# Performance work log

Measured on AMD Instinct MI355X. Metric: run time of the kernel, lower is better.

## Reference

```python
import jax, jax.numpy as jnp
import numpy as np

B, S, E, H = 8, 2048, 512, 4
D = E // H


def setup_inputs() -> dict:
    key = jax.random.key(0)
    ks = jax.random.split(key, 9)
    std = 0.05  # keras 'normal' initializer default stddev
    return {
        "x": jax.random.normal(ks[0], (B, S, E), dtype=jnp.float32),
        "Wq": jax.random.normal(ks[1], (E, E), dtype=jnp.float32) * std,
        "Wk": jax.random.normal(ks[2], (E, E), dtype=jnp.float32) * std,
        "Wv": jax.random.normal(ks[3], (E, E), dtype=jnp.float32) * std,
        "Wepi": jax.random.normal(ks[4], (S, S), dtype=jnp.float32) * std,
        "bq": jax.random.normal(ks[5], (S, 1), dtype=jnp.float32) * std,
        "bk": jax.random.normal(ks[6], (S, 1), dtype=jnp.float32) * std,
        "bv": jax.random.normal(ks[7], (S, 1), dtype=jnp.float32) * std,
        "bo": jax.random.normal(ks[8], (S, 1), dtype=jnp.float32) * std,
    }


def reference(x, Wq, Wk, Wv, Wepi, bq, bk, bv, bo):
    b, s, e = x.shape
    # QKV projections; [S,1] biases broadcast across the feature dim
    q = x @ Wq + bq  # [B,S,E]
    k = x @ Wk + bk
    v = x @ Wv + bv
    # split heads -> [B,H,S,D]
    q = q.reshape(b, s, H, D).transpose(0, 2, 1, 3)
    k = k.reshape(b, s, H, D).transpose(0, 2, 1, 3)
    v = v.reshape(b, s, H, D).transpose(0, 2, 1, 3)
    # NOTE: source scales by sqrt(seq_length), not sqrt(head_dim)
    scale = 1.0 / np.sqrt(float(s)).astype(np.float32)
    scores = jnp.einsum("bhsd,bhtd->bhst", q, k) * scale  # [B,H,S,S]
    attn = jax.nn.softmax(scores, axis=-1)
    # epigenomic multiplicative mask applied AFTER softmax (broadcast [S,S])
    attn = attn * Wepi
    effect = jnp.einsum("bhst,bhtd->bhsd", attn, v)  # [B,H,S,D]
    effect = effect.transpose(0, 2, 1, 3).reshape(b, s, e) + bo
    # original returns attention in merged-batch layout [B*H, S, S]
    return effect, attn.reshape(b * H, s, s)
```

## Files before the change

kernel.cpp:

```cpp
#include <hip/hip_runtime.h>
#include <hip/hip_bf16.h>

constexpr int Bn = 8, Sn = 2048, En = 512, Hn = 4, Dn = 128;
constexpr int BHn = Bn * Hn;
constexpr int Mqkv = Bn * Sn;

typedef __attribute__((ext_vector_type(8))) short short8;
typedef __attribute__((ext_vector_type(4))) float f32x4;

__device__ __forceinline__ unsigned short f2bf(float f) {
  unsigned int u = __builtin_bit_cast(unsigned int, f);
  u += 0x7FFF + ((u >> 16) & 1);
  return (unsigned short)(u >> 16);
}

__device__ __forceinline__ void bar_pub() {
  asm volatile("s_waitcnt lgkmcnt(0)" ::: "memory");
  __builtin_amdgcn_s_barrier();
  asm volatile("" ::: "memory");
}

__global__ __launch_bounds__(256) void qkv_kernel(
    const float* __restrict__ x, const float* __restrict__ Wq,
    const float* __restrict__ Wk, const float* __restrict__ Wv,
    const float* __restrict__ bq, const float* __restrict__ bk,
    const float* __restrict__ bv, unsigned short* __restrict__ qkv) {
  const int z = blockIdx.z;
  const float* W = (z == 0) ? Wq : (z == 1 ? Wk : Wv);
  const float* bias = (z == 0) ? bq : (z == 1 ? bk : bv);
  unsigned short* out = qkv + (size_t)z * BHn * Sn * Dn;

  __shared__ unsigned short As[128][40];
  __shared__ unsigned short BsT[128][40];

  const int t = threadIdx.x;
  const int l = t & 63, w = t >> 6;
  const int wm = w >> 1, wn = w & 1;
  const int m0 = blockIdx.x * 128, n0 = blockIdx.y * 128;

  f32x4 acc[4][4] = {};

  for (int k0 = 0; k0 < En; k0 += 32) {
    __syncthreads();
#pragma unroll
    for (int i = 0; i < 4; ++i) {
      int idx = t + i * 256;
      int row = idx >> 3, c4 = (idx & 7) * 4;
      float4 v = *reinterpret_cast<const float4*>(&x[(size_t)(m0 + row) * En + k0 + c4]);
      ushort4 p;
      p.x = f2bf(v.x); p.y = f2bf(v.y); p.z = f2bf(v.z); p.w = f2bf(v.w);
      *reinterpret_cast<ushort4*>(&As[row][c4]) = p;
    }
#pragma unroll
    for (int i = 0; i < 4; ++i) {
      int idx = t + i * 256;
      int kk = idx >> 5, c4 = (idx & 31) * 4;
      float4 v = *reinterpret_cast<const float4*>(&W[(size_t)(k0 + kk) * En + n0 + c4]);
      BsT[c4 + 0][kk] = f2bf(v.x);
      BsT[c4 + 1][kk] = f2bf(v.y);
      BsT[c4 + 2][kk] = f2bf(v.z);
      BsT[c4 + 3][kk] = f2bf(v.w);
    }
    __syncthreads();

    const int koff = (l >> 4) * 8;
    short8 a[4], bfr[4];
#pragma unroll
    for (int m = 0; m < 4; ++m)
      a[m] = *reinterpret_cast<const short8*>(&As[wm * 64 + m * 16 + (l & 15)][koff]);
#pragma unroll
    for (int n = 0; n < 4; ++n)
      bfr[n] = *reinterpret_cast<const short8*>(&BsT[wn * 64 + n * 16 + (l & 15)][koff]);
#pragma unroll
    for (int m = 0; m < 4; ++m)
#pragma unroll
      for (int n = 0; n < 4; ++n)
        acc[m][n] = __builtin_amdgcn_mfma_f32_16x16x32_bf16(a[m], bfr[n], acc[m][n], 0, 0, 0);
  }

#pragma unroll
  for (int m = 0; m < 4; ++m)
#pragma unroll
    for (int n = 0; n < 4; ++n)
#pragma unroll
      for (int j = 0; j < 4; ++j) {
        int row = m0 + wm * 64 + m * 16 + (l >> 4) * 4 + j;
        int col = n0 + wn * 64 + n * 16 + (l & 15);
        int s = row & (Sn - 1);
        float v = acc[m][n][j] + bias[s];
        int b = row >> 11;
        int h = col >> 7, d = col & 127;
        out[(size_t)((b * Hn + h) * Sn + s) * Dn + d] = f2bf(v);
      }
}

__global__ __launch_bounds__(256) void vtrans_kernel(
    const unsigned short* __restrict__ v, unsigned short* __restrict__ vT) {
  const int s0 = blockIdx.x * 64, d0 = blockIdx.y * 64;
  const int bh = blockIdx.z;
  const unsigned short* vp = v + (size_t)bh * Sn * Dn;
  unsigned short* op = vT + (size_t)bh * Dn * Sn;
  __shared__ unsigned short Ls[64][72];
  const int t = threadIdx.x;
#pragma unroll
  for (int it = 0; it < 2; ++it) {
    int flat = t + it * 256;
    int r = flat >> 3, cc = flat & 7;
    *reinterpret_cast<short8*>(&Ls[r][cc * 8]) =
        *reinterpret_cast<const short8*>(&vp[(size_t)(s0 + r) * Dn + d0 + cc * 8]);
  }
  __syncthreads();
#pragma unroll
  for (int it = 0; it < 2; ++it) {
    int flat = t + it * 256;
    int d = flat >> 3, sc = flat & 7;
    short8 o;
#pragma unroll
    for (int jo = 0; jo < 8; ++jo) {
      int jj = (jo + sc) & 7;
      o[jj] = (short)Ls[sc * 8 + jj][d];
    }
    *reinterpret_cast<short8*>(&op[(size_t)(d0 + d) * Sn + s0 + sc * 8]) = o;
  }
}

__global__ __launch_bounds__(256, 4) void fused_attn8_kernel(
    const unsigned short* __restrict__ qkv, const unsigned short* __restrict__ vT,
    const float* __restrict__ Wepi, const float* __restrict__ bo,
    float* __restrict__ attn, float* __restrict__ effect) {
  const int id = blockIdx.x;
  const int s0 = ((id & 7) * 4 + ((id >> 3) & 3)) * 64;
  const int bh = id >> 5;

  const unsigned short* qp = qkv + (size_t)bh * Sn * Dn;
  const unsigned short* kp = qkv + (size_t)(BHn + bh) * Sn * Dn;
  const unsigned short* vt = vT + (size_t)bh * Dn * Sn;

  __shared__ unsigned short Kb[2][32 * 128];
  __shared__ unsigned short Vs[128 * 40];
  __shared__ float Sf[64 * 36];
  __shared__ unsigned short Ps[64 * 40];

  const int t = threadIdx.x, l = t & 63, w = t >> 6;
  const int g = l >> 4, i = l & 15;
  const int th = w & 1, sh = w >> 1;
  const float scale = 0.022097086912079608f;

  short8 aq[2][4];
#pragma unroll
  for (int sf = 0; sf < 2; ++sf)
#pragma unroll
    for (int ks = 0; ks < 4; ++ks)
      aq[sf][ks] = *reinterpret_cast<const short8*>(
          &qp[(size_t)(s0 + sh * 32 + sf * 16 + i) * Dn + ks * 32 + g * 8]);

  int ksrc[2], kdst[2], vsrc[2], vdst[2];
#pragma unroll
  for (int it = 0; it < 2; ++it) {
    int flat = t + it * 256;
    int r = flat >> 4, cc = flat & 15;
    ksrc[it] = r * Dn + cc * 8;
    kdst[it] = r * 128 + ((cc ^ (r & 15)) << 3);
    int dr = flat >> 2, t8 = (flat & 3) * 8;
    vsrc[it] = dr * Sn + t8;
    vdst[it] = dr * 40 + t8;
  }

  const int sr = t >> 3, cc4 = (t & 7) * 4;

  short8 kreg[2];
#pragma unroll
  for (int it = 0; it < 2; ++it)
    kreg[it] = *reinterpret_cast<const short8*>(&kp[ksrc[it]]);
#pragma unroll
  for (int it = 0; it < 2; ++it)
    *reinterpret_cast<short8*>(&Kb[0][kdst[it]]) = kreg[it];
#pragma unroll
  for (int it = 0; it < 2; ++it)
    kreg[it] = *reinterpret_cast<const short8*>(&kp[(size_t)32 * Dn + ksrc[it]]);
  bar_pub();

  float rs[2] = {0.f, 0.f};
  for (int kt = 0; kt < 64; ++kt) {
    const int b = kt & 1;
    f32x4 accT[2] = {};
    __builtin_amdgcn_s_setprio(1);
#pragma unroll
    for (int ks = 0; ks < 4; ++ks) {
      short8 ak = *reinterpret_cast<const short8*>(
          &Kb[b][(th * 16 + i) * 128 + (((ks * 4 + g) ^ i) << 3)]);
#pragma unroll
      for (int sf = 0; sf < 2; ++sf)
        accT[sf] = __builtin_amdgcn_mfma_f32_16x16x32_bf16(ak, aq[sf][ks], accT[sf], 0, 0, 0);
    }
    __builtin_amdgcn_s_setprio(0);
#pragma unroll
    for (int sf = 0; sf < 2; ++sf)
      rs[sf] += __expf(accT[sf][0] * scale) + __expf(accT[sf][1] * scale) +
                __expf(accT[sf][2] * scale) + __expf(accT[sf][3] * scale);
    if (kt < 63) {
#pragma unroll
      for (int it = 0; it < 2; ++it)
        *reinterpret_cast<short8*>(&Kb[b ^ 1][kdst[it]]) = kreg[it];
      if (kt < 62)
#pragma unroll
        for (int it = 0; it < 2; ++it)
          kreg[it] = *reinterpret_cast<const short8*>(
              &kp[(size_t)(kt + 2) * 32 * Dn + ksrc[it]]);
    }
    bar_pub();
  }

  float* red = reinterpret_cast<float*>(Ps);
#pragma unroll
  for (int sf = 0; sf < 2; ++sf) {
    float v = rs[sf];
    v += __shfl_xor(v, 16);
    v += __shfl_xor(v, 32);
    if (l < 16) red[w * 32 + sf * 16 + l] = v;
  }
  bar_pub();
  if (g == 0 && th == 0) {
#pragma unroll
    for (int sf = 0; sf < 2; ++sf) {
      const int s = sh * 32 + sf * 16 + i;
      float sum = red[w * 32 + sf * 16 + i] + red[(w ^ 1) * 32 + sf * 16 + i];
      Sf[s * 36 + 32] = 1.0f / sum;
    }
  }

  short8 vld[2];
#pragma unroll
  for (int it = 0; it < 2; ++it)
    kreg[it] = *reinterpret_cast<const short8*>(&kp[ksrc[it]]);
#pragma unroll
  for (int it = 0; it < 2; ++it)
    *reinterpret_cast<short8*>(&Kb[0][kdst[it]]) = kreg[it];
#pragma unroll
  for (int it = 0; it < 2; ++it) {
    kreg[it] = *reinterpret_cast<const short8*>(&kp[(size_t)32 * Dn + ksrc[it]]);
    vld[it] = *reinterpret_cast<const short8*>(&vt[vsrc[it]]);
  }
  bar_pub();

  float* attnb = attn + (size_t)bh * Sn * Sn;
  const float* wp0 = Wepi + (size_t)(s0 + sr) * Sn + cc4;
  const float* wp1 = Wepi + (size_t)(s0 + sr + 32) * Sn + cc4;
  float* ap0 = attnb + (size_t)(s0 + sr) * Sn + cc4;
  float* ap1 = attnb + (size_t)(s0 + sr + 32) * Sn + cc4;

  f32x4 pv[4][2] = {};
  for (int kt = 0; kt < 64; ++kt) {
    const int b = kt & 1;
    const int t0 = kt * 32;
    float4 wq0 = *reinterpret_cast<const float4*>(&wp0[t0]);
    float4 wq1 = *reinterpret_cast<const float4*>(&wp1[t0]);

    f32x4 accT[2] = {};
    __builtin_amdgcn_s_setprio(1);
#pragma unroll
    for (int ks = 0; ks < 4; ++ks) {
      short8 ak = *reinterpret_cast<const short8*>(
          &Kb[b][(th * 16 + i) * 128 + (((ks * 4 + g) ^ i) << 3)]);
#pragma unroll
      for (int sf = 0; sf < 2; ++sf)
        accT[sf] = __builtin_amdgcn_mfma_f32_16x16x32_bf16(ak, aq[sf][ks], accT[sf], 0, 0, 0);
    }
    if (kt > 0) {
#pragma unroll
      for (int pf = 0; pf < 4; ++pf) {
        short8 pa = *reinterpret_cast<const short8*>(&Ps[(pf * 16 + i) * 40 + g * 8]);
#pragma unroll
        for (int nf = 0; nf < 2; ++nf) {
          const int d = w * 32 + nf * 16 + i;
          short8 bv = *reinterpret_cast<const short8*>(&Vs[d * 40 + g * 8]);
          pv[pf][nf] = __builtin_amdgcn_mfma_f32_16x16x32_bf16(pa, bv, pv[pf][nf], 0, 0, 0);
        }
      }
    }
    __builtin_amdgcn_s_setprio(0);

#pragma unroll
    for (int sf = 0; sf < 2; ++sf)
      *reinterpret_cast<f32x4*>(
          &Sf[(sh * 32 + sf * 16 + i) * 36 + th * 16 + g * 4]) = accT[sf];
    bar_pub();

    if (kt < 63)
#pragma unroll
      for (int it = 0; it < 2; ++it)
        *reinterpret_cast<short8*>(&Kb[b ^ 1][kdst[it]]) = kreg[it];
#pragma unroll
    for (int it = 0; it < 2; ++it)
      *reinterpret_cast<short8*>(&Vs[vdst[it]]) = vld[it];
    if (kt < 62)
#pragma unroll
      for (int it = 0; it < 2; ++it)
        kreg[it] = *reinterpret_cast<const short8*>(
            &kp[(size_t)(kt + 2) * 32 * Dn + ksrc[it]]);
    if (kt < 63)
#pragma unroll
      for (int it = 0; it < 2; ++it)
        vld[it] = *reinterpret_cast<const short8*>(&vt[t0 + 32 + vsrc[it]]);

    {
      float4 s4 = *reinterpret_cast<const float4*>(&Sf[sr * 36 + cc4]);
      float iv0 = Sf[sr * 36 + 32];
      f32x4 o0;
      o0[0] = __expf(s4.x * scale) * iv0 * wq0.x;
      o0[1] = __expf(s4.y * scale) * iv0 * wq0.y;
      o0[2] = __expf(s4.z * scale) * iv0 * wq0.z;
      o0[3] = __expf(s4.w * scale) * iv0 * wq0.w;
      __builtin_nontemporal_store(o0, reinterpret_cast<f32x4*>(&ap0[t0]));
      ushort4 pk0;
      pk0.x = f2bf(o0[0]); pk0.y = f2bf(o0[1]); pk0.z = f2bf(o0[2]); pk0.w = f2bf(o0[3]);
      *reinterpret_cast<ushort4*>(&Ps[sr * 40 + cc4]) = pk0;

      float4 s5 = *reinterpret_cast<const float4*>(&Sf[(sr + 32) * 36 + cc4]);
      float iv1 = Sf[(sr + 32) * 36 + 32];
      f32x4 o1;
      o1[0] = __expf(s5.x * scale) * iv1 * wq1.x;
      o1[1] = __expf(s5.y * scale) * iv1 * wq1.y;
      o1[2] = __expf(s5.z * scale) * iv1 * wq1.z;
      o1[3] = __expf(s5.w * scale) * iv1 * wq1.w;
      __builtin_nontemporal_store(o1, reinterpret_cast<f32x4*>(&ap1[t0]));
      ushort4 pk1;
      pk1.x = f2bf(o1[0]); pk1.y = f2bf(o1[1]); pk1.z = f2bf(o1[2]); pk1.w = f2bf(o1[3]);
      *reinterpret_cast<ushort4*>(&Ps[(sr + 32) * 40 + cc4]) = pk1;
    }
    bar_pub();
  }

  __builtin_amdgcn_s_setprio(1);
#pragma unroll
  for (int pf = 0; pf < 4; ++pf) {
    short8 pa = *reinterpret_cast<const short8*>(&Ps[(pf * 16 + i) * 40 + g * 8]);
#pragma unroll
    for (int nf = 0; nf < 2; ++nf) {
      const int d = w * 32 + nf * 16 + i;
      short8 bv = *reinterpret_cast<const short8*>(&Vs[d * 40 + g * 8]);
      pv[pf][nf] = __builtin_amdgcn_mfma_f32_16x16x32_bf16(pa, bv, pv[pf][nf], 0, 0, 0);
    }
  }
  __builtin_amdgcn_s_setprio(0);

  const int b_ = bh >> 2, h_ = bh & 3;
#pragma unroll
  for (int pf = 0; pf < 4; ++pf)
#pragma unroll
    for (int j = 0; j < 4; ++j) {
      const int row = s0 + pf * 16 + g * 4 + j;
      const float bias = bo[row];
#pragma unroll
      for (int nf = 0; nf < 2; ++nf)
        __builtin_nontemporal_store(
            pv[pf][nf][j] + bias,
            &effect[(size_t)(b_ * Sn + row) * En + h_ * Dn + w * 32 + nf * 16 + i]);
    }
}

extern "C" void kernel_launch(void* const* d_in, const int* in_sizes, int n_in,
                              void* d_out, int out_size, void* d_ws, size_t ws_size,
                              hipStream_t stream) {
  const float* x    = (const float*)d_in[0];
  const float* Wq   = (const float*)d_in[1];
  const float* Wk   = (const float*)d_in[2];
  const float* Wv   = (const float*)d_in[3];
  const float* Wepi = (const float*)d_in[4];
  const float* bq   = (const float*)d_in[5];
  const float* bk   = (const float*)d_in[6];
  const float* bv   = (const float*)d_in[7];
  const float* bo   = (const float*)d_in[8];

  float* effect = (float*)d_out;
  float* attn = effect + (size_t)Bn * Sn * En;
  unsigned short* qkv = (unsigned short*)d_ws;
  unsigned short* vT = qkv + (size_t)3 * BHn * Sn * Dn;

  qkv_kernel<<<dim3(Mqkv / 128, En / 128, 3), 256, 0, stream>>>(x, Wq, Wk, Wv, bq, bk, bv, qkv);
  vtrans_kernel<<<dim3(Sn / 64, Dn / 64, BHn), 256, 0, stream>>>(
      qkv + (size_t)2 * BHn * Sn * Dn, vT);
  fused_attn8_kernel<<<dim3(1024), 256, 0, stream>>>(qkv, vT, Wepi, bo, attn, effect);
}
```

Measured before the change: 349.4 us.

## Single-buffer K in LDS, load V fragments directly to registers, raise occupancy

Replaces the double-buffered K tile with a single buffer and an extra barrier per iteration. It also drops the V shared-memory staging in favour of loading each wave's V^T MFMA fragments straight from global memory into registers. Launch bounds go from 4 to 6 waves-per-EU so more blocks fit per CU with the smaller LDS footprint. The trade is an extra barrier per iteration and exposed global-load latency on V, in exchange for less LDS traffic and more occupancy.

```diff
diff --git a/kernel.cpp b/kernel.cpp
--- a/kernel.cpp
+++ b/kernel.cpp
@@ -124,7 +124,7 @@
   }
 }
 
-__global__ __launch_bounds__(256, 4) void fused_attn8_kernel(
+__global__ __launch_bounds__(256, 6) void fused_attn11_kernel(
     const unsigned short* __restrict__ qkv, const unsigned short* __restrict__ vT,
     const float* __restrict__ Wepi, const float* __restrict__ bo,
     float* __restrict__ attn, float* __restrict__ effect) {
@@ -136,8 +136,7 @@
   const unsigned short* kp = qkv + (size_t)(BHn + bh) * Sn * Dn;
   const unsigned short* vt = vT + (size_t)bh * Dn * Sn;
 
-  __shared__ unsigned short Kb[2][32 * 128];
-  __shared__ unsigned short Vs[128 * 40];
+  __shared__ unsigned short Kb[32 * 128];
   __shared__ float Sf[64 * 36];
   __shared__ unsigned short Ps[64 * 40];
 
@@ -154,16 +153,13 @@
       aq[sf][ks] = *reinterpret_cast<const short8*>(
           &qp[(size_t)(s0 + sh * 32 + sf * 16 + i) * Dn + ks * 32 + g * 8]);
 
-  int ksrc[2], kdst[2], vsrc[2], vdst[2];
+  int ksrc[2], kdst[2];
 #pragma unroll
   for (int it = 0; it < 2; ++it) {
     int flat = t + it * 256;
     int r = flat >> 4, cc = flat & 15;
     ksrc[it] = r * Dn + cc * 8;
     kdst[it] = r * 128 + ((cc ^ (r & 15)) << 3);
-    int dr = flat >> 2, t8 = (flat & 3) * 8;
-    vsrc[it] = dr * Sn + t8;
-    vdst[it] = dr * 40 + t8;
   }
 
   const int sr = t >> 3, cc4 = (t & 7) * 4;
@@ -174,7 +170,7 @@
     kreg[it] = *reinterpret_cast<const short8*>(&kp[ksrc[it]]);
 #pragma unroll
   for (int it = 0; it < 2; ++it)
-    *reinterpret_cast<short8*>(&Kb[0][kdst[it]]) = kreg[it];
+    *reinterpret_cast<short8*>(&Kb[kdst[it]]) = kreg[it];
 #pragma unroll
   for (int it = 0; it < 2; ++it)
     kreg[it] = *reinterpret_cast<const short8*>(&kp[(size_t)32 * Dn + ksrc[it]]);
@@ -182,13 +178,12 @@
 
   float rs[2] = {0.f, 0.f};
   for (int kt = 0; kt < 64; ++kt) {
-    const int b = kt & 1;
     f32x4 accT[2] = {};
     __builtin_amdgcn_s_setprio(1);
 #pragma unroll
     for (int ks = 0; ks < 4; ++ks) {
       short8 ak = *reinterpret_cast<const short8*>(
-          &Kb[b][(th * 16 + i) * 128 + (((ks * 4 + g) ^ i) << 3)]);
+          &Kb[(th * 16 + i) * 128 + (((ks * 4 + g) ^ i) << 3)]);
 #pragma unroll
       for (int sf = 0; sf < 2; ++sf)
         accT[sf] = __builtin_amdgcn_mfma_f32_16x16x32_bf16(ak, aq[sf][ks], accT[sf], 0, 0, 0);
@@ -198,10 +193,11 @@
     for (int sf = 0; sf < 2; ++sf)
       rs[sf] += __expf(accT[sf][0] * scale) + __expf(accT[sf][1] * scale) +
                 __expf(accT[sf][2] * scale) + __expf(accT[sf][3] * scale);
+    bar_pub();
     if (kt < 63) {
 #pragma unroll
       for (int it = 0; it < 2; ++it)
-        *reinterpret_cast<short8*>(&Kb[b ^ 1][kdst[it]]) = kreg[it];
+        *reinterpret_cast<short8*>(&Kb[kdst[it]]) = kreg[it];
       if (kt < 62)
 #pragma unroll
         for (int it = 0; it < 2; ++it)
@@ -229,18 +225,21 @@
     }
   }
 
-  short8 vld[2];
 #pragma unroll
   for (int it = 0; it < 2; ++it)
     kreg[it] = *reinterpret_cast<const short8*>(&kp[ksrc[it]]);
-#pragma unroll
-  for (int it = 0; it < 2; ++it)
-    *reinterpret_cast<short8*>(&Kb[0][kdst[it]]) = kreg[it];
-#pragma unroll
-  for (int it = 0; it < 2; ++it) {
+  bar_pub();
+#pragma unroll
+  for (int it = 0; it < 2; ++it)
+    *reinterpret_cast<short8*>(&Kb[kdst[it]]) = kreg[it];
+#pragma unroll
+  for (int it = 0; it < 2; ++it)
     kreg[it] = *reinterpret_cast<const short8*>(&kp[(size_t)32 * Dn + ksrc[it]]);
-    vld[it] = *reinterpret_cast<const short8*>(&vt[vsrc[it]]);
-  }
+  short8 vreg[2];
+#pragma unroll
+  for (int nf = 0; nf < 2; ++nf)
+    vreg[nf] = *reinterpret_cast<const short8*>(
+        &vt[(size_t)(w * 32 + nf * 16 + i) * Sn + g * 8]);
   bar_pub();
 
   float* attnb = attn + (size_t)bh * Sn * Sn;
@@ -251,7 +250,6 @@
 
   f32x4 pv[4][2] = {};
   for (int kt = 0; kt < 64; ++kt) {
-    const int b = kt & 1;
     const int t0 = kt * 32;
     float4 wq0 = *reinterpret_cast<const float4*>(&wp0[t0]);
     float4 wq1 = *reinterpret_cast<const float4*>(&wp1[t0]);
@@ -261,7 +259,7 @@
 #pragma unroll
     for (int ks = 0; ks < 4; ++ks) {
       short8 ak = *reinterpret_cast<const short8*>(
-          &Kb[b][(th * 16 + i) * 128 + (((ks * 4 + g) ^ i) << 3)]);
+          &Kb[(th * 16 + i) * 128 + (((ks * 4 + g) ^ i) << 3)]);
 #pragma unroll
       for (int sf = 0; sf < 2; ++sf)
         accT[sf] = __builtin_amdgcn_mfma_f32_16x16x32_bf16(ak, aq[sf][ks], accT[sf], 0, 0, 0);
@@ -271,14 +269,17 @@
       for (int pf = 0; pf < 4; ++pf) {
         short8 pa = *reinterpret_cast<const short8*>(&Ps[(pf * 16 + i) * 40 + g * 8]);
 #pragma unroll
-        for (int nf = 0; nf < 2; ++nf) {
-          const int d = w * 32 + nf * 16 + i;
-          short8 bv = *reinterpret_cast<const short8*>(&Vs[d * 40 + g * 8]);
-          pv[pf][nf] = __builtin_amdgcn_mfma_f32_16x16x32_bf16(pa, bv, pv[pf][nf], 0, 0, 0);
-        }
+        for (int nf = 0; nf < 2; ++nf)
+          pv[pf][nf] = __builtin_amdgcn_mfma_f32_16x16x32_bf16(pa, vreg[nf], pv[pf][nf], 0, 0, 0);
       }
     }
     __builtin_amdgcn_s_setprio(0);
+
+    if (kt > 0)
+#pragma unroll
+      for (int nf = 0; nf < 2; ++nf)
+        vreg[nf] = *reinterpret_cast<const short8*>(
+            &vt[(size_t)(w * 32 + nf * 16 + i) * Sn + t0 + g * 8]);
 
 #pragma unroll
     for (int sf = 0; sf < 2; ++sf)
@@ -286,22 +287,16 @@
           &Sf[(sh * 32 + sf * 16 + i) * 36 + th * 16 + g * 4]) = accT[sf];
     bar_pub();
 
-    if (kt < 63)
+    if (kt < 63) {
 #pragma unroll
       for (int it = 0; it < 2; ++it)
-        *reinterpret_cast<short8*>(&Kb[b ^ 1][kdst[it]]) = kreg[it];
-#pragma unroll
-    for (int it = 0; it < 2; ++it)
-      *reinterpret_cast<short8*>(&Vs[vdst[it]]) = vld[it];
-    if (kt < 62)
-#pragma unroll
-      for (int it = 0; it < 2; ++it)
-        kreg[it] = *reinterpret_cast<const short8*>(
-            &kp[(size_t)(kt + 2) * 32 * Dn + ksrc[it]]);
-    if (kt < 63)
-#pragma unroll
-      for (int it = 0; it < 2; ++it)
-        vld[it] = *reinterpret_cast<const short8*>(&vt[t0 + 32 + vsrc[it]]);
+        *reinterpret_cast<short8*>(&Kb[kdst[it]]) = kreg[it];
+      if (kt < 62)
+#pragma unroll
+        for (int it = 0; it < 2; ++it)
+          kreg[it] = *reinterpret_cast<const short8*>(
+              &kp[(size_t)(kt + 2) * 32 * Dn + ksrc[it]]);
+    }
 
     {
       float4 s4 = *reinterpret_cast<const float4*>(&Sf[sr * 36 + cc4]);
@@ -336,11 +331,8 @@
   for (int pf = 0; pf < 4; ++pf) {
     short8 pa = *reinterpret_cast<const short8*>(&Ps[(pf * 16 + i) * 40 + g * 8]);
 #pragma unroll
-    for (int nf = 0; nf < 2; ++nf) {
-      const int d = w * 32 + nf * 16 + i;
-      short8 bv = *reinterpret_cast<const short8*>(&Vs[d * 40 + g * 8]);
-      pv[pf][nf] = __builtin_amdgcn_mfma_f32_16x16x32_bf16(pa, bv, pv[pf][nf], 0, 0, 0);
-    }
+    for (int nf = 0; nf < 2; ++nf)
+      pv[pf][nf] = __builtin_amdgcn_mfma_f32_16x16x32_bf16(pa, vreg[nf], pv[pf][nf], 0, 0, 0);
   }
   __builtin_amdgcn_s_setprio(0);
 
@@ -380,5 +372,5 @@
   qkv_kernel<<<dim3(Mqkv / 128, En / 128, 3), 256, 0, stream>>>(x, Wq, Wk, Wv, bq, bk, bv, qkv);
   vtrans_kernel<<<dim3(Sn / 64, Dn / 64, BHn), 256, 0, stream>>>(
       qkv + (size_t)2 * BHn * Sn * Dn, vT);
-  fused_attn8_kernel<<<dim3(1024), 256, 0, stream>>>(qkv, vT, Wepi, bo, attn, effect);
-}
+  fused_attn11_kernel<<<dim3(1024), 256, 0, stream>>>(qkv, vT, Wepi, bo, attn, effect);
+}
```

Result: slower. 754.3 us (+115.9%).
